# Kernel tuning notes

Measured on AMD Instinct MI355X. Metric: run time of the kernel, lower is better.

Reference implementation:

```python
import jax, jax.numpy as jnp
import numpy as np

# ---- physics constraint targets (constants, precomputed with numpy) ----
_ARC = np.array([[-1,-1,-1],[2,2,2],[-1,-1,-1]], np.float32)
_CURV5 = np.array([[0,0,-1,0,0],[0,-1,2,-1,0],[-1,2,4,2,-1],[0,-1,2,-1,0],[0,0,-1,0,0]], np.float32)
_RAD = np.array([[0,-1,0],[-1,4,-1],[0,-1,0]], np.float32)
_TAN = np.array([[-1,0,-1],[0,4,0],[-1,0,-1]], np.float32)

def _bilinear_1d(a, out_n):
    # torch F.interpolate bilinear, align_corners=False, along axis 0
    n = a.shape[0]
    src = (np.arange(out_n) + 0.5) * n / out_n - 0.5
    i0 = np.clip(np.floor(src).astype(int), 0, n - 1)
    i1 = np.clip(i0 + 1, 0, n - 1)
    f = np.clip(src - np.floor(src), 0.0, 1.0).astype(np.float32)
    shp = (out_n,) + (1,) * (a.ndim - 1)
    return a[i0] * (1 - f).reshape(shp) + a[i1] * f.reshape(shp)

_CURV3 = _bilinear_1d(_bilinear_1d(_CURV5, 3).T, 3).T  # 5x5 -> 3x3 separable bilinear
CONSTRAINTS = jnp.asarray(np.stack([_ARC, _CURV3, _RAD, _TAN]))  # [4,3,3]

NUM_HEADS = 4
PHYSICS_WEIGHT = 0.1


def setup_inputs() -> dict:
    key = jax.random.key(0)
    ks = jax.random.split(key, 6)
    B, N, C = 8, 1024, 256
    return {
        "x": jax.random.normal(ks[0], (B, N, C), jnp.float32),
        "qkv_w": jax.random.normal(ks[1], (3 * C, C), jnp.float32) * (C ** -0.5),
        "qkv_b": jax.random.normal(ks[2], (3 * C,), jnp.float32) * 0.02,
        "proj_w": jax.random.normal(ks[3], (C, C), jnp.float32) * (C ** -0.5),
        "proj_b": jax.random.normal(ks[4], (C,), jnp.float32) * 0.02,
        "kernels": jax.random.normal(ks[5], (4, 3, 3), jnp.float32) * 0.1,
        "H": 32,
        "W": 32,
    }


def _physics_prior(x, kernels, H, W):
    # Original: depthwise conv each channel with each kernel, mean over kernels,
    # mean over channels, sigmoid, outer product. Conv + means are linear, so
    # mean-over-kernels and mean-over-channels commute with the (shared-kernel)
    # depthwise conv: conv(mean_C(x), mean_k(kernels)).
    B, N, C = x.shape
    xm = x.mean(axis=2).reshape(B, 1, H, W)            # [B,1,H,W]
    kmean = kernels.mean(axis=0)[None, None]           # [1,1,3,3] (OIHW)
    conv = jax.lax.conv_general_dilated(
        xm, kmean, window_strides=(1, 1), padding=((1, 1), (1, 1)),
        dimension_numbers=("NCHW", "OIHW", "NCHW"))
    amap = jax.nn.sigmoid(conv.reshape(B, N))          # [B,N]
    return amap[:, :, None] * amap[:, None, :]         # [B,N,N]


def _reg_loss(kernels):
    mse = jnp.mean((kernels - CONSTRAINTS) ** 2, axis=(1, 2)).sum()
    l1 = 0.01 * jnp.abs(kernels).sum()
    return mse + l1


def reference(x, qkv_w, qkv_b, proj_w, proj_b, kernels, H, W):
    B, N, C = x.shape
    hd = C // NUM_HEADS
    scale = hd ** -0.5
    qkv = (x @ qkv_w.T + qkv_b).reshape(B, N, 3, NUM_HEADS, hd)
    qkv = qkv.transpose(2, 0, 3, 1, 4)                 # [3,B,h,N,hd]
    q, k, v = qkv[0], qkv[1], qkv[2]
    attn = jnp.einsum("bhnd,bhmd->bhnm", q, k) * scale  # [B,h,N,N]
    prior = _physics_prior(x, kernels, H, W)            # [B,N,N]
    attn = attn + PHYSICS_WEIGHT * prior[:, None]
    attn = jax.nn.softmax(attn, axis=-1)                # dropout: eval mode (identity)
    out = jnp.einsum("bhnm,bhmd->bhnd", attn, v)
    out = out.transpose(0, 2, 1, 3).reshape(B, N, C)
    out = out @ proj_w.T + proj_b
    attention_weights = attn.mean(axis=1)               # [B,N,N]
    return out, attention_weights, _reg_loss(kernels)
```

## Files before the change

### kernel.cpp

```cpp
#include <hip/hip_runtime.h>
#include <cstdint>

typedef _Float16 h16;
typedef __attribute__((ext_vector_type(8))) _Float16 f16x8;
typedef __attribute__((ext_vector_type(4))) _Float16 f16x4;
typedef __attribute__((ext_vector_type(4))) float f32x4;

#define L2E 1.44269504f
#define QSCALE (0.125f * L2E)

__global__ void k_cast(const float* __restrict__ x, const float* __restrict__ qw,
                       const float* __restrict__ pw, h16* __restrict__ xh,
                       h16* __restrict__ qwh, h16* __restrict__ pwh,
                       float* __restrict__ xm) {
  int bid = blockIdx.x, tid = threadIdx.x;
  if (bid < 2048) {
    int i4 = bid * 256 + tid;
    float4 v = ((const float4*)x)[i4];
    f16x4 o = {(h16)v.x, (h16)v.y, (h16)v.z, (h16)v.w};
    ((f16x4*)xh)[i4] = o;
    float s = v.x + v.y + v.z + v.w;
#pragma unroll
    for (int off = 32; off; off >>= 1) s += __shfl_xor(s, off);
    if ((tid & 63) == 0) xm[i4 >> 6] = s * (1.0f / 256.0f);
  } else {
    int i4 = (bid - 2048) * 256 + tid;
    if (i4 < 49152) {
      float4 v = ((const float4*)qw)[i4];
      f16x4 o = {(h16)v.x, (h16)v.y, (h16)v.z, (h16)v.w};
      ((f16x4*)qwh)[i4] = o;
    } else {
      int j = i4 - 49152;
      float4 v = ((const float4*)pw)[j];
      f16x4 o = {(h16)v.x, (h16)v.y, (h16)v.z, (h16)v.w};
      ((f16x4*)pwh)[j] = o;
    }
  }
}

__global__ void k_amap(const float* __restrict__ xm,
                       const float* __restrict__ kern,
                       float* __restrict__ amap) {
  int idx = blockIdx.x * 256 + threadIdx.x;
  int b = idx >> 10, n = idx & 1023;
  int y = n >> 5, xq = n & 31;
  float km[9];
#pragma unroll
  for (int i = 0; i < 9; ++i)
    km[i] = 0.25f * (kern[i] + kern[9 + i] + kern[18 + i] + kern[27 + i]);
  float acc = 0.f;
#pragma unroll
  for (int dy = 0; dy < 3; ++dy) {
#pragma unroll
    for (int dx = 0; dx < 3; ++dx) {
      int yy = y + dy - 1, xx = xq + dx - 1;
      if (yy >= 0 && yy < 32 && xx >= 0 && xx < 32)
        acc += km[dy * 3 + dx] * xm[(b << 10) + (yy << 5) + xx];
    }
  }
  amap[idx] = 1.0f / (1.0f + __expf(-acc));
}

__global__ __launch_bounds__(128) void k_qkv(
    const h16* __restrict__ xh, const h16* __restrict__ qwh,
    const float* __restrict__ bias, h16* __restrict__ Qh,
    h16* __restrict__ Kh, h16* __restrict__ Vt) {
  const int w = threadIdx.x >> 6, lane = threadIdx.x & 63;
  const int g = lane >> 4, li = lane & 15;
  const int tile = blockIdx.x * 2 + w;
  const int tr = tile & 255, tc = tile >> 8;
  const int r0 = tr * 32, c0 = tc * 64;
  f32x4 acc[2][4];
#pragma unroll
  for (int mr = 0; mr < 2; ++mr)
#pragma unroll
    for (int nc = 0; nc < 4; ++nc) acc[mr][nc] = {0.f, 0.f, 0.f, 0.f};
  for (int ks = 0; ks < 8; ++ks) {
    int k0 = ks * 32 + g * 8;
    f16x8 a[2], bf[4];
#pragma unroll
    for (int mr = 0; mr < 2; ++mr)
      a[mr] = *(const f16x8*)(xh + (size_t)(r0 + mr * 16 + li) * 256 + k0);
#pragma unroll
    for (int nc = 0; nc < 4; ++nc)
      bf[nc] = *(const f16x8*)(qwh + (size_t)(c0 + nc * 16 + li) * 256 + k0);
#pragma unroll
    for (int mr = 0; mr < 2; ++mr)
#pragma unroll
      for (int nc = 0; nc < 4; ++nc)
        acc[mr][nc] = __builtin_amdgcn_mfma_f32_16x16x32_f16(a[mr], bf[nc],
                                                             acc[mr][nc], 0, 0, 0);
  }
  const int which = c0 >> 8;
  const int hh = (c0 >> 6) & 3;
  const int bq = r0 >> 10;
  const size_t base = ((size_t)(bq * 4 + hh)) << 16;
  if (which == 2) {
#pragma unroll
    for (int nc = 0; nc < 4; ++nc) {
      int d = nc * 16 + li;
      float bv = bias[c0 + d];
#pragma unroll
      for (int mr = 0; mr < 2; ++mr) {
        int n0 = (r0 & 1023) + mr * 16 + g * 4;
        f16x4 pk = {(h16)(acc[mr][nc][0] + bv), (h16)(acc[mr][nc][1] + bv),
                    (h16)(acc[mr][nc][2] + bv), (h16)(acc[mr][nc][3] + bv)};
        *(f16x4*)(Vt + base + (size_t)d * 1024 + n0) = pk;
      }
    }
  } else {
    h16* dst = (which == 0) ? Qh : Kh;
#pragma unroll
    for (int nc = 0; nc < 4; ++nc) {
      int d = nc * 16 + li;
      float bv = bias[c0 + d];
#pragma unroll
      for (int mr = 0; mr < 2; ++mr) {
#pragma unroll
        for (int r = 0; r < 4; ++r) {
          int n = (r0 & 1023) + mr * 16 + g * 4 + r;
          dst[base + (size_t)n * 64 + d] = (h16)(acc[mr][nc][r] + bv);
        }
      }
    }
  }
}

__global__ void k_knorm(const h16* __restrict__ Kh, float* __restrict__ Kmaxb) {
  __shared__ float red[4];
  const int tid = threadIdx.x;
  const h16* base = Kh + ((size_t)blockIdx.x << 16);
  float mx = 0.f;
#pragma unroll
  for (int i = 0; i < 4; ++i) {
    int n = i * 256 + tid;
    float s2 = 0.f;
#pragma unroll
    for (int ks = 0; ks < 8; ++ks) {
      f16x8 v = *(const f16x8*)(base + (size_t)n * 64 + ks * 8);
#pragma unroll
      for (int e = 0; e < 8; ++e) {
        float f = (float)v[e];
        s2 += f * f;
      }
    }
    mx = fmaxf(mx, s2);
  }
#pragma unroll
  for (int off = 32; off; off >>= 1) mx = fmaxf(mx, __shfl_xor(mx, off));
  if ((tid & 63) == 0) red[tid >> 6] = mx;
  __syncthreads();
  if (tid == 0) {
    mx = fmaxf(fmaxf(red[0], red[1]), fmaxf(red[2], red[3]));
    Kmaxb[blockIdx.x] = sqrtf(mx);
  }
}

__global__ __launch_bounds__(256, 4) void k_lsum(
    const h16* __restrict__ Qh, const h16* __restrict__ Kh,
    const float* __restrict__ amap, const float* __restrict__ Kmaxb,
    float* __restrict__ Erow) {
  __shared__ float am_s[1024];
  __shared__ float Lsh[2][2][16];
  const int tid = threadIdx.x;
  const int wave = tid >> 6, lane = tid & 63, g = lane >> 4, li = lane & 15;
  const int qsub = wave >> 1, jh = wave & 1;
  const int bh = blockIdx.x >> 5, rt = blockIdx.x & 31;
  const int b = bh >> 2;
  const int r0 = rt * 32 + qsub * 16;
  const size_t base = ((size_t)bh) << 16;

  am_s[tid] = amap[(b << 10) + tid];
  am_s[tid + 256] = amap[(b << 10) + 256 + tid];
  am_s[tid + 512] = amap[(b << 10) + 512 + tid];
  am_s[tid + 768] = amap[(b << 10) + 768 + tid];
  __syncthreads();

  f16x8 qf[2];
#pragma unroll
  for (int ks = 0; ks < 2; ++ks)
    qf[ks] = *(const f16x8*)(Qh + base + (size_t)(r0 + li) * 64 + ks * 32 + g * 8);

  float nq2 = 0.f;
#pragma unroll
  for (int ks = 0; ks < 2; ++ks)
#pragma unroll
    for (int e = 0; e < 8; ++e) {
      float f = (float)qf[ks][e];
      nq2 += f * f;
    }
  nq2 += __shfl_xor(nq2, 16);
  nq2 += __shfl_xor(nq2, 32);
  const float c = 0.125f * sqrtf(nq2) * Kmaxb[bh] + 0.11f;
  const float mcl = -c * L2E;
  const float amr2 = 0.1f * L2E * am_s[r0 + li];
  const int prow = ((li >> 2) << 3) + (li & 3);

  float lpart = 0.f;
  for (int jj = 0; jj < 8; ++jj) {
    const int j0 = jh * 512 + jj * 64;
#pragma unroll
    for (int u = 0; u < 2; ++u) {
#pragma unroll
      for (int ab = 0; ab < 2; ++ab) {
        const int rK = j0 + u * 32 + ab * 4 + prow;
        f16x8 k0 = *(const f16x8*)(Kh + base + (size_t)rK * 64 + g * 8);
        f16x8 k1 = *(const f16x8*)(Kh + base + (size_t)rK * 64 + 32 + g * 8);
        f32x4 s = {0.f, 0.f, 0.f, 0.f};
        s = __builtin_amdgcn_mfma_f32_16x16x32_f16(k0, qf[0], s, 0, 0, 0);
        s = __builtin_amdgcn_mfma_f32_16x16x32_f16(k1, qf[1], s, 0, 0, 0);
        f32x4 am4 = *(const f32x4*)&am_s[j0 + u * 32 + g * 8 + ab * 4];
#pragma unroll
        for (int r = 0; r < 4; ++r) {
          float pre = fmaf(amr2, am4[r], mcl);
          lpart += exp2f(fmaf(s[r], QSCALE, pre));
        }
      }
    }
  }
  lpart += __shfl_xor(lpart, 16);
  lpart += __shfl_xor(lpart, 32);
  if (g == 0) Lsh[qsub][jh][li] = lpart;
  __syncthreads();
  if (jh == 0 && g == 0) {
    float l = Lsh[qsub][0][li] + Lsh[qsub][1][li];
    Erow[((size_t)bh << 10) + r0 + li] = c * L2E + __log2f(l);
  }
}

__global__ __launch_bounds__(512, 4) void k_attn(
    const h16* __restrict__ Qh, const h16* __restrict__ Kh,
    const h16* __restrict__ Vt, const float* __restrict__ amap,
    const float* __restrict__ Erow, float* __restrict__ AW,
    h16* __restrict__ OHh) {
  __shared__ float am_s[1024];
  __shared__ __align__(16) unsigned char Pst[8][2048];
  __shared__ float Osh[4][16][68];

  const int tid = threadIdx.x;
  const int wave = tid >> 6, lane = tid & 63, g = lane >> 4, li = lane & 15;
  const int h = wave >> 1, jh = wave & 1;
  const int b = blockIdx.x & 7, rt = blockIdx.x >> 3;
  const int r0 = rt * 16;
  const int bh = b * 4 + h;
  const size_t base = ((size_t)bh) << 16;

  am_s[tid] = amap[(b << 10) + tid];
  am_s[tid + 512] = amap[(b << 10) + 512 + tid];
  __syncthreads();

  f16x8 qf[2];
#pragma unroll
  for (int ks = 0; ks < 2; ++ks)
    qf[ks] = *(const f16x8*)(Qh + base + (size_t)(r0 + li) * 64 + ks * 32 + g * 8);

  const float E = Erow[((size_t)bh << 10) + r0 + li];
  const float amr2 = 0.1f * L2E * am_s[r0 + li];
  const int prow = ((li >> 2) << 3) + (li & 3);
  const int swz = (li & 7) << 4;

  f32x4 o[4];
#pragma unroll
  for (int nd = 0; nd < 4; ++nd) o[nd] = {0.f, 0.f, 0.f, 0.f};

  const int arow = tid >> 5, ac = (tid & 31) << 2;
  const int ahalf = ac >> 6, aci = ac & 63;
  const int aswz = (arow & 7) << 4;

  for (int jj = 0; jj < 8; ++jj) {
    const int j0 = jh * 512 + jj * 64;
    f16x8 bfrag[2];
#pragma unroll
    for (int u = 0; u < 2; ++u) {
      f32x4 s[2];
      f32x4 am4[2];
#pragma unroll
      for (int ab = 0; ab < 2; ++ab) {
        const int rK = j0 + u * 32 + ab * 4 + prow;
        f16x8 k0 = *(const f16x8*)(Kh + base + (size_t)rK * 64 + g * 8);
        f16x8 k1 = *(const f16x8*)(Kh + base + (size_t)rK * 64 + 32 + g * 8);
        f32x4 a = {0.f, 0.f, 0.f, 0.f};
        a = __builtin_amdgcn_mfma_f32_16x16x32_f16(k0, qf[0], a, 0, 0, 0);
        a = __builtin_amdgcn_mfma_f32_16x16x32_f16(k1, qf[1], a, 0, 0, 0);
        s[ab] = a;
        am4[ab] = *(const f32x4*)&am_s[j0 + u * 32 + g * 8 + ab * 4];
      }
      f16x8 bf;
#pragma unroll
      for (int ab = 0; ab < 2; ++ab)
#pragma unroll
        for (int r = 0; r < 4; ++r) {
          float pre = fmaf(amr2, am4[ab][r], -E);
          bf[ab * 4 + r] = (h16)exp2f(fmaf(s[ab][r], QSCALE, pre));
        }
      bfrag[u] = bf;
      *(f16x8*)(&Pst[wave][(li << 7) + ((u * 64 + g * 16) ^ swz)]) = bf;
    }
#pragma unroll
    for (int nd = 0; nd < 4; ++nd) {
      f16x8 v0 = *(const f16x8*)(Vt + base + (size_t)(nd * 16 + li) * 1024 + j0 + g * 8);
      f16x8 v1 = *(const f16x8*)(Vt + base + (size_t)(nd * 16 + li) * 1024 + j0 + 32 + g * 8);
      o[nd] = __builtin_amdgcn_mfma_f32_16x16x32_f16(v0, bfrag[0], o[nd], 0, 0, 0);
      o[nd] = __builtin_amdgcn_mfma_f32_16x16x32_f16(v1, bfrag[1], o[nd], 0, 0, 0);
    }
    __syncthreads();
    {
      float s0 = 0.f, s1 = 0.f, s2 = 0.f, s3 = 0.f;
#pragma unroll
      for (int h2 = 0; h2 < 4; ++h2) {
        f16x4 v = *(const f16x4*)(&Pst[h2 * 2 + ahalf][(arow << 7) + ((aci * 2) ^ aswz)]);
        s0 += (float)v[0]; s1 += (float)v[1]; s2 += (float)v[2]; s3 += (float)v[3];
      }
      const int colg = ahalf * 512 + jj * 64 + aci;
      float4 ov = {0.25f * s0, 0.25f * s1, 0.25f * s2, 0.25f * s3};
      *(float4*)(AW + ((size_t)b << 20) + (size_t)(r0 + arow) * 1024 + colg) = ov;
    }
    __syncthreads();
  }
  if (jh == 1) {
#pragma unroll
    for (int nd = 0; nd < 4; ++nd)
      *(f32x4*)&Osh[h][li][nd * 16 + g * 4] = o[nd];
  }
  __syncthreads();
  if (jh == 0) {
#pragma unroll
    for (int nd = 0; nd < 4; ++nd) {
      f32x4 p = *(const f32x4*)&Osh[h][li][nd * 16 + g * 4];
      f16x4 pk = {(h16)(o[nd][0] + p[0]), (h16)(o[nd][1] + p[1]),
                  (h16)(o[nd][2] + p[2]), (h16)(o[nd][3] + p[3])};
      *(f16x4*)(OHh + (size_t)((b << 10) + r0 + li) * 256 + h * 64 + nd * 16 + g * 4) = pk;
    }
  }
}

__global__ __launch_bounds__(128) void k_proj(const h16* __restrict__ OHh,
                                              const h16* __restrict__ pwh,
                                              const float* __restrict__ bias,
                                              float* __restrict__ out) {
  const int w = threadIdx.x >> 6, lane = threadIdx.x & 63;
  const int g = lane >> 4, li = lane & 15;
  const int tile = blockIdx.x * 2 + w;
  const int tc = tile & 3, tr = tile >> 2;
  const int r0 = tr * 32, c0 = tc * 64;
  f32x4 acc[2][4];
#pragma unroll
  for (int mr = 0; mr < 2; ++mr)
#pragma unroll
    for (int nc = 0; nc < 4; ++nc) acc[mr][nc] = {0.f, 0.f, 0.f, 0.f};
  for (int ks = 0; ks < 8; ++ks) {
    int k0 = ks * 32 + g * 8;
    f16x8 a[2], bf[4];
#pragma unroll
    for (int mr = 0; mr < 2; ++mr)
      a[mr] = *(const f16x8*)(OHh + (size_t)(r0 + mr * 16 + li) * 256 + k0);
#pragma unroll
    for (int nc = 0; nc < 4; ++nc)
      bf[nc] = *(const f16x8*)(pwh + (size_t)(c0 + nc * 16 + li) * 256 + k0);
#pragma unroll
    for (int mr = 0; mr < 2; ++mr)
#pragma unroll
      for (int nc = 0; nc < 4; ++nc)
        acc[mr][nc] = __builtin_amdgcn_mfma_f32_16x16x32_f16(a[mr], bf[nc],
                                                             acc[mr][nc], 0, 0, 0);
  }
#pragma unroll
  for (int nc = 0; nc < 4; ++nc) {
    int cc = c0 + nc * 16 + li;
    float bv = bias[cc];
#pragma unroll
    for (int mr = 0; mr < 2; ++mr)
#pragma unroll
      for (int r = 0; r < 4; ++r) {
        int m = r0 + mr * 16 + g * 4 + r;
        out[(size_t)m * 256 + cc] = acc[mr][nc][r] + bv;
      }
  }
}

__global__ void k_reg(const float* __restrict__ kern, float* __restrict__ out) {
  const float Cst[36] = {
      -1.f, -1.f, -1.f, 2.f, 2.f, 2.f, -1.f, -1.f, -1.f,
      -0.11111111f, 0.f, -0.11111111f, 0.f, 4.f, 0.f,
      -0.11111111f, 0.f, -0.11111111f,
      0.f, -1.f, 0.f, -1.f, 4.f, -1.f, 0.f, -1.f, 0.f,
      -1.f, 0.f, -1.f, 0.f, 4.f, 0.f, -1.f, 0.f, -1.f};
  int t = threadIdx.x;
  float v = 0.f;
  if (t < 36) {
    float kv = kern[t];
    float d = kv - Cst[t];
    v = d * d * (1.0f / 9.0f) + 0.01f * fabsf(kv);
  }
#pragma unroll
  for (int off = 32; off; off >>= 1) v += __shfl_xor(v, off);
  if (t == 0) out[0] = v;
}

extern "C" void kernel_launch(void* const* d_in, const int* in_sizes, int n_in,
                              void* d_out, int out_size, void* d_ws,
                              size_t ws_size, hipStream_t stream) {
  const float* x = (const float*)d_in[0];
  const float* qkv_w = (const float*)d_in[1];
  const float* qkv_b = (const float*)d_in[2];
  const float* proj_w = (const float*)d_in[3];
  const float* proj_b = (const float*)d_in[4];
  const float* kern = (const float*)d_in[5];

  float* out = (float*)d_out;
  float* aw = out + 2097152;
  float* rl = out + 10485760;

  float* xm = (float*)d_ws;
  float* amap = xm + 8192;
  float* Erow = amap + 8192;
  float* Kmaxb = Erow + 32768;
  h16* xh = (h16*)(Kmaxb + 64);
  h16* qwh = xh + 2097152;
  h16* pwh = qwh + 196608;
  h16* Qh = pwh + 65536;
  h16* Kh = Qh + 2097152;
  h16* Vt = Kh + 2097152;
  h16* OHh = Vt + 2097152;

  k_cast<<<2304, 256, 0, stream>>>(x, qkv_w, proj_w, xh, qwh, pwh, xm);
  k_amap<<<32, 256, 0, stream>>>(xm, kern, amap);
  k_qkv<<<1536, 128, 0, stream>>>(xh, qwh, qkv_b, Qh, Kh, Vt);
  k_knorm<<<32, 256, 0, stream>>>(Kh, Kmaxb);
  k_lsum<<<1024, 256, 0, stream>>>(Qh, Kh, amap, Kmaxb, Erow);
  k_attn<<<512, 512, 0, stream>>>(Qh, Kh, Vt, amap, Erow, aw, OHh);
  k_proj<<<512, 128, 0, stream>>>(OHh, pwh, proj_b, out);
  k_reg<<<1, 64, 0, stream>>>(kern, rl);
}
```

Before: 219.8 us.

## Fuse row-sum pass into attention kernel and process two key tiles per sync

Merges the separate log-sum-exp kernel into the attention kernel: each block first computes the softmax denominator for its rows, then reuses the same Q fragments and block layout to compute probabilities, PV, and the head-averaged attention weights. This removes one launch and the Erow round trip through global memory. The attention loop also handles two 64-key tiles per iteration, halving the number of barrier pairs, and writes 8-wide attention-weight stores. In exchange, the shared-memory staging buffer doubles and the output-reduction buffer now aliases it, and the fused kernel still reads K twice.

Result: faster. 215.0 us (-2.2%).

```diff
diff --git a/kernel.cpp b/kernel.cpp
--- a/kernel.cpp
+++ b/kernel.cpp
@@ -156,24 +156,25 @@
   }
 }
 
-__global__ __launch_bounds__(256, 4) void k_lsum(
+__global__ __launch_bounds__(512, 4) void k_fattn(
     const h16* __restrict__ Qh, const h16* __restrict__ Kh,
-    const float* __restrict__ amap, const float* __restrict__ Kmaxb,
-    float* __restrict__ Erow) {
+    const h16* __restrict__ Vt, const float* __restrict__ amap,
+    const float* __restrict__ Kmaxb, float* __restrict__ AW,
+    h16* __restrict__ OHh) {
   __shared__ float am_s[1024];
-  __shared__ float Lsh[2][2][16];
+  __shared__ float Lsh[4][2][16];
+  __shared__ __align__(16) unsigned char Pst[8][2][2048];
+
   const int tid = threadIdx.x;
   const int wave = tid >> 6, lane = tid & 63, g = lane >> 4, li = lane & 15;
-  const int qsub = wave >> 1, jh = wave & 1;
-  const int bh = blockIdx.x >> 5, rt = blockIdx.x & 31;
-  const int b = bh >> 2;
-  const int r0 = rt * 32 + qsub * 16;
+  const int h = wave >> 1, jh = wave & 1;
+  const int b = blockIdx.x & 7, rt = blockIdx.x >> 3;
+  const int r0 = rt * 16;
+  const int bh = b * 4 + h;
   const size_t base = ((size_t)bh) << 16;
 
   am_s[tid] = amap[(b << 10) + tid];
-  am_s[tid + 256] = amap[(b << 10) + 256 + tid];
   am_s[tid + 512] = amap[(b << 10) + 512 + tid];
-  am_s[tid + 768] = amap[(b << 10) + 768 + tid];
   __syncthreads();
 
   f16x8 qf[2];
@@ -195,6 +196,7 @@
   const float mcl = -c * L2E;
   const float amr2 = 0.1f * L2E * am_s[r0 + li];
   const int prow = ((li >> 2) << 3) + (li & 3);
+  const int swz = (li & 7) << 4;
 
   float lpart = 0.f;
   for (int jj = 0; jj < 8; ++jj) {
@@ -211,125 +213,104 @@
         s = __builtin_amdgcn_mfma_f32_16x16x32_f16(k1, qf[1], s, 0, 0, 0);
         f32x4 am4 = *(const f32x4*)&am_s[j0 + u * 32 + g * 8 + ab * 4];
 #pragma unroll
-        for (int r = 0; r < 4; ++r) {
-          float pre = fmaf(amr2, am4[r], mcl);
-          lpart += exp2f(fmaf(s[r], QSCALE, pre));
-        }
+        for (int r = 0; r < 4; ++r)
+          lpart += exp2f(fmaf(s[r], QSCALE, fmaf(amr2, am4[r], mcl)));
       }
     }
   }
   lpart += __shfl_xor(lpart, 16);
   lpart += __shfl_xor(lpart, 32);
-  if (g == 0) Lsh[qsub][jh][li] = lpart;
+  if (lane < 16) Lsh[h][jh][li] = lpart;
   __syncthreads();
-  if (jh == 0 && g == 0) {
-    float l = Lsh[qsub][0][li] + Lsh[qsub][1][li];
-    Erow[((size_t)bh << 10) + r0 + li] = c * L2E + __log2f(l);
-  }
-}
-
-__global__ __launch_bounds__(512, 4) void k_attn(
-    const h16* __restrict__ Qh, const h16* __restrict__ Kh,
-    const h16* __restrict__ Vt, const float* __restrict__ amap,
-    const float* __restrict__ Erow, float* __restrict__ AW,
-    h16* __restrict__ OHh) {
-  __shared__ float am_s[1024];
-  __shared__ __align__(16) unsigned char Pst[8][2048];
-  __shared__ float Osh[4][16][68];
-
-  const int tid = threadIdx.x;
-  const int wave = tid >> 6, lane = tid & 63, g = lane >> 4, li = lane & 15;
-  const int h = wave >> 1, jh = wave & 1;
-  const int b = blockIdx.x & 7, rt = blockIdx.x >> 3;
-  const int r0 = rt * 16;
-  const int bh = b * 4 + h;
-  const size_t base = ((size_t)bh) << 16;
-
-  am_s[tid] = amap[(b << 10) + tid];
-  am_s[tid + 512] = amap[(b << 10) + 512 + tid];
-  __syncthreads();
-
-  f16x8 qf[2];
-#pragma unroll
-  for (int ks = 0; ks < 2; ++ks)
-    qf[ks] = *(const f16x8*)(Qh + base + (size_t)(r0 + li) * 64 + ks * 32 + g * 8);
-
-  const float E = Erow[((size_t)bh << 10) + r0 + li];
-  const float amr2 = 0.1f * L2E * am_s[r0 + li];
-  const int prow = ((li >> 2) << 3) + (li & 3);
-  const int swz = (li & 7) << 4;
+  const float E = c * L2E + __log2f(Lsh[h][0][li] + Lsh[h][1][li]);
 
   f32x4 o[4];
 #pragma unroll
   for (int nd = 0; nd < 4; ++nd) o[nd] = {0.f, 0.f, 0.f, 0.f};
 
-  const int arow = tid >> 5, ac = (tid & 31) << 2;
-  const int ahalf = ac >> 6, aci = ac & 63;
-  const int aswz = (arow & 7) << 4;
-
-  for (int jj = 0; jj < 8; ++jj) {
-    const int j0 = jh * 512 + jj * 64;
-    f16x8 bfrag[2];
-#pragma unroll
-    for (int u = 0; u < 2; ++u) {
-      f32x4 s[2];
-      f32x4 am4[2];
-#pragma unroll
-      for (int ab = 0; ab < 2; ++ab) {
-        const int rK = j0 + u * 32 + ab * 4 + prow;
-        f16x8 k0 = *(const f16x8*)(Kh + base + (size_t)rK * 64 + g * 8);
-        f16x8 k1 = *(const f16x8*)(Kh + base + (size_t)rK * 64 + 32 + g * 8);
-        f32x4 a = {0.f, 0.f, 0.f, 0.f};
-        a = __builtin_amdgcn_mfma_f32_16x16x32_f16(k0, qf[0], a, 0, 0, 0);
-        a = __builtin_amdgcn_mfma_f32_16x16x32_f16(k1, qf[1], a, 0, 0, 0);
-        s[ab] = a;
-        am4[ab] = *(const f32x4*)&am_s[j0 + u * 32 + g * 8 + ab * 4];
-      }
-      f16x8 bf;
-#pragma unroll
-      for (int ab = 0; ab < 2; ++ab)
-#pragma unroll
-        for (int r = 0; r < 4; ++r) {
-          float pre = fmaf(amr2, am4[ab][r], -E);
-          bf[ab * 4 + r] = (h16)exp2f(fmaf(s[ab][r], QSCALE, pre));
+  const int ar = tid >> 5, ac8 = (tid & 31) << 3;
+  const int ahalf = ac8 >> 7, ajj = (ac8 >> 6) & 1, acin = ac8 & 63;
+  const int aswz = (ar & 7) << 4;
+
+  for (int pj = 0; pj < 4; ++pj) {
+    f16x8 bf[2][2];
+#pragma unroll
+    for (int q2 = 0; q2 < 2; ++q2) {
+      const int j0 = jh * 512 + (pj * 2 + q2) * 64;
+#pragma unroll
+      for (int u = 0; u < 2; ++u) {
+        f32x4 s[2];
+        f32x4 am4[2];
+#pragma unroll
+        for (int ab = 0; ab < 2; ++ab) {
+          const int rK = j0 + u * 32 + ab * 4 + prow;
+          f16x8 k0 = *(const f16x8*)(Kh + base + (size_t)rK * 64 + g * 8);
+          f16x8 k1 = *(const f16x8*)(Kh + base + (size_t)rK * 64 + 32 + g * 8);
+          f32x4 a = {0.f, 0.f, 0.f, 0.f};
+          a = __builtin_amdgcn_mfma_f32_16x16x32_f16(k0, qf[0], a, 0, 0, 0);
+          a = __builtin_amdgcn_mfma_f32_16x16x32_f16(k1, qf[1], a, 0, 0, 0);
+          s[ab] = a;
+          am4[ab] = *(const f32x4*)&am_s[j0 + u * 32 + g * 8 + ab * 4];
         }
-      bfrag[u] = bf;
-      *(f16x8*)(&Pst[wave][(li << 7) + ((u * 64 + g * 16) ^ swz)]) = bf;
+        f16x8 pk;
+#pragma unroll
+        for (int ab = 0; ab < 2; ++ab)
+#pragma unroll
+          for (int r = 0; r < 4; ++r)
+            pk[ab * 4 + r] =
+                (h16)exp2f(fmaf(s[ab][r], QSCALE, fmaf(amr2, am4[ab][r], -E)));
+        bf[q2][u] = pk;
+        *(f16x8*)(&Pst[wave][q2][(li << 7) + ((u * 64 + g * 16) ^ swz)]) = pk;
+      }
     }
 #pragma unroll
     for (int nd = 0; nd < 4; ++nd) {
-      f16x8 v0 = *(const f16x8*)(Vt + base + (size_t)(nd * 16 + li) * 1024 + j0 + g * 8);
-      f16x8 v1 = *(const f16x8*)(Vt + base + (size_t)(nd * 16 + li) * 1024 + j0 + 32 + g * 8);
-      o[nd] = __builtin_amdgcn_mfma_f32_16x16x32_f16(v0, bfrag[0], o[nd], 0, 0, 0);
-      o[nd] = __builtin_amdgcn_mfma_f32_16x16x32_f16(v1, bfrag[1], o[nd], 0, 0, 0);
+      const h16* vb = Vt + base + (size_t)(nd * 16 + li) * 1024;
+#pragma unroll
+      for (int q2 = 0; q2 < 2; ++q2) {
+        const int j0 = jh * 512 + (pj * 2 + q2) * 64;
+        f16x8 v0 = *(const f16x8*)(vb + j0 + g * 8);
+        f16x8 v1 = *(const f16x8*)(vb + j0 + 32 + g * 8);
+        o[nd] = __builtin_amdgcn_mfma_f32_16x16x32_f16(v0, bf[q2][0], o[nd], 0, 0, 0);
+        o[nd] = __builtin_amdgcn_mfma_f32_16x16x32_f16(v1, bf[q2][1], o[nd], 0, 0, 0);
+      }
     }
     __syncthreads();
     {
       float s0 = 0.f, s1 = 0.f, s2 = 0.f, s3 = 0.f;
+      float s4 = 0.f, s5 = 0.f, s6 = 0.f, s7 = 0.f;
 #pragma unroll
       for (int h2 = 0; h2 < 4; ++h2) {
-        f16x4 v = *(const f16x4*)(&Pst[h2 * 2 + ahalf][(arow << 7) + ((aci * 2) ^ aswz)]);
+        f16x8 v = *(const f16x8*)(&Pst[h2 * 2 + ahalf][ajj][(ar << 7) +
+                                                           ((acin * 2) ^ aswz)]);
         s0 += (float)v[0]; s1 += (float)v[1]; s2 += (float)v[2]; s3 += (float)v[3];
-      }
-      const int colg = ahalf * 512 + jj * 64 + aci;
-      float4 ov = {0.25f * s0, 0.25f * s1, 0.25f * s2, 0.25f * s3};
-      *(float4*)(AW + ((size_t)b << 20) + (size_t)(r0 + arow) * 1024 + colg) = ov;
+        s4 += (float)v[4]; s5 += (float)v[5]; s6 += (float)v[6]; s7 += (float)v[7];
+      }
+      const int colg = ahalf * 512 + (pj * 2 + ajj) * 64 + acin;
+      float* dst = AW + ((size_t)b << 20) + (size_t)(r0 + ar) * 1024 + colg;
+      float4 o1 = {0.25f * s0, 0.25f * s1, 0.25f * s2, 0.25f * s3};
+      float4 o2 = {0.25f * s4, 0.25f * s5, 0.25f * s6, 0.25f * s7};
+      *(float4*)dst = o1;
+      *(float4*)(dst + 4) = o2;
     }
     __syncthreads();
   }
+
+  float* Osh = (float*)&Pst[0][0][0];
   if (jh == 1) {
 #pragma unroll
     for (int nd = 0; nd < 4; ++nd)
-      *(f32x4*)&Osh[h][li][nd * 16 + g * 4] = o[nd];
+      *(f32x4*)&Osh[((h * 16 + li) << 6) + nd * 16 + g * 4] = o[nd];
   }
   __syncthreads();
   if (jh == 0) {
 #pragma unroll
     for (int nd = 0; nd < 4; ++nd) {
-      f32x4 p = *(const f32x4*)&Osh[h][li][nd * 16 + g * 4];
+      f32x4 p = *(const f32x4*)&Osh[((h * 16 + li) << 6) + nd * 16 + g * 4];
       f16x4 pk = {(h16)(o[nd][0] + p[0]), (h16)(o[nd][1] + p[1]),
                   (h16)(o[nd][2] + p[2]), (h16)(o[nd][3] + p[3])};
-      *(f16x4*)(OHh + (size_t)((b << 10) + r0 + li) * 256 + h * 64 + nd * 16 + g * 4) = pk;
+      *(f16x4*)(OHh + (size_t)((b << 10) + r0 + li) * 256 + h * 64 + nd * 16 +
+                g * 4) = pk;
     }
   }
 }
@@ -413,8 +394,7 @@
 
   float* xm = (float*)d_ws;
   float* amap = xm + 8192;
-  float* Erow = amap + 8192;
-  float* Kmaxb = Erow + 32768;
+  float* Kmaxb = amap + 8192;
   h16* xh = (h16*)(Kmaxb + 64);
   h16* qwh = xh + 2097152;
   h16* pwh = qwh + 196608;
@@ -427,8 +407,7 @@
   k_amap<<<32, 256, 0, stream>>>(xm, kern, amap);
   k_qkv<<<1536, 128, 0, stream>>>(xh, qwh, qkv_b, Qh, Kh, Vt);
   k_knorm<<<32, 256, 0, stream>>>(Kh, Kmaxb);
-  k_lsum<<<1024, 256, 0, stream>>>(Qh, Kh, amap, Kmaxb, Erow);
-  k_attn<<<512, 512, 0, stream>>>(Qh, Kh, Vt, amap, Erow, aw, OHh);
+  k_fattn<<<512, 512, 0, stream>>>(Qh, Kh, Vt, amap, Kmaxb, aw, OHh);
   k_proj<<<512, 128, 0, stream>>>(OHh, pwh, proj_b, out);
   k_reg<<<1, 64, 0, stream>>>(kern, rl);
 }
```
